# Kernel tuning notes

Measured on AMD Instinct MI355X. Metric: run time of the kernel, lower is better.

Reference implementation:

```python
import jax, jax.numpy as jnp
import numpy as np

B_SZ, T, D = 4, 8192, 512

def setup_inputs() -> dict:
    key = jax.random.key(0)
    k1, k2, k3, k4 = jax.random.split(key, 4)
    x = jax.random.normal(k1, (B_SZ, T, D), dtype=jnp.float32)
    # nn.Linear(dim, dim, bias=False) weights, applied as x @ W.T
    W_B = jax.random.normal(k2, (D, D), dtype=jnp.float32) * (1.0 / np.sqrt(D))
    W_C = jax.random.normal(k3, (D, D), dtype=jnp.float32) * (1.0 / np.sqrt(D))
    A = jax.random.normal(k4, (D,), dtype=jnp.float32)
    return {"x": x, "W_B": W_B, "W_C": W_C, "A": A}

def reference(x, W_B, W_C, A):
    # b: [B, T, D]
    b = jnp.einsum('btd,ed->bte', x, W_B)
    a = jax.nn.sigmoid(A)  # [D], diagonal decay per channel

    def step(h, b_t):
        h = a * h + b_t  # [B, D]
        return h, h

    h0 = jnp.zeros_like(b[:, 0])
    _, outs = jax.lax.scan(step, h0, jnp.swapaxes(b, 0, 1))  # outs: [T, B, D]
    outputs = jnp.swapaxes(outs, 0, 1)  # [B, T, D]
    return jnp.einsum('btd,ed->bte', outputs, W_C)
```

## Files before the change

kernel.cpp:

```cpp
#include <hip/hip_runtime.h>
#include <hip/hip_bf16.h>
#include <stdint.h>

#define B_SZ 4
#define T_LEN 8192
#define D_DIM 512
#define M_TOT 32768
#define RB 64
#define NCH 128
#define SCS 516

typedef __attribute__((ext_vector_type(8))) short bf16x8v;
typedef __attribute__((ext_vector_type(4))) float f32x4v;

__device__ __forceinline__ unsigned short f2bf(float f) {
  unsigned int u = __float_as_uint(f);
  u += 0x7fffu + ((u >> 16) & 1u);
  return (unsigned short)(u >> 16);
}
__device__ __forceinline__ float bf2f(unsigned short b) {
  return __uint_as_float(((unsigned int)b) << 16);
}
__device__ __forceinline__ float sigmoidf_(float x) { return 1.0f / (1.0f + expf(-x)); }

__device__ __forceinline__ bf16x8v pack8(float4 a, float4 b) {
  union { unsigned u[4]; bf16x8v v; } r;
  r.u[0] = (unsigned)f2bf(a.x) | ((unsigned)f2bf(a.y) << 16);
  r.u[1] = (unsigned)f2bf(a.z) | ((unsigned)f2bf(a.w) << 16);
  r.u[2] = (unsigned)f2bf(b.x) | ((unsigned)f2bf(b.y) << 16);
  r.u[3] = (unsigned)f2bf(b.z) | ((unsigned)f2bf(b.w) << 16);
  return r.v;
}

__global__ void prep_k(const float* __restrict__ Wb, const float* __restrict__ Wc,
                       const float* __restrict__ A, unsigned short* __restrict__ wpk,
                       unsigned short* __restrict__ papk) {
  const int b = blockIdx.x;
  const int tid = threadIdx.x;
  if (b == 64) {
#pragma unroll
    for (int s = 0; s < 2; ++s) {
      int ch = s * 256 + tid;
      float a = sigmoidf_(A[ch]);
      float p = a;
      int lhi = ((ch >> 3) & 3) << 4;
      int e = ch & 7;
      int csl = ch >> 5;
      for (int row = 0; row < RB; ++row) {
        int chunk = (row >> 4) * 16 + csl;
        int lane = (row & 15) | lhi;
        papk[chunk * 512 + lane * 8 + e] = f2bf(p);
        p *= a;
      }
    }
    return;
  }
  __shared__ unsigned short sd[16 * 520];
  const float* src = (b < 32) ? Wb + (size_t)b * 8192 : Wc + (size_t)(b - 32) * 8192;
  unsigned short* dst =
      (b < 32) ? wpk + (size_t)b * 8192 : wpk + 262144 + (size_t)(b - 32) * 8192;
#pragma unroll
  for (int it = 0; it < 4; ++it) {
    int idx = (it * 256 + tid) * 8;
    int row = idx >> 9, col = idx & 511;
    float4 v0 = *(const float4*)&src[row * 512 + col];
    float4 v1 = *(const float4*)&src[row * 512 + col + 4];
    uint4 o;
    o.x = (unsigned)f2bf(v0.x) | ((unsigned)f2bf(v0.y) << 16);
    o.y = (unsigned)f2bf(v0.z) | ((unsigned)f2bf(v0.w) << 16);
    o.z = (unsigned)f2bf(v1.x) | ((unsigned)f2bf(v1.y) << 16);
    o.w = (unsigned)f2bf(v1.z) | ((unsigned)f2bf(v1.w) << 16);
    *(uint4*)&sd[row * 520 + col] = o;
  }
  __syncthreads();
#pragma unroll
  for (int it = 0; it < 4; ++it) {
    int idx = it * 256 + tid;
    int cs = idx >> 6, l = idx & 63;
    uint4 v = *(const uint4*)&sd[(l & 15) * 520 + cs * 32 + (l >> 4) * 8];
    *(uint4*)&dst[(size_t)cs * 512 + l * 8] = v;
  }
}

__global__ void carry_k(const float* __restrict__ A, float* __restrict__ cst) {
  const int ch = threadIdx.x;
  const int bi = blockIdx.x;
  float a = sigmoidf_(A[ch]);
  float p = a;
#pragma unroll
  for (int i = 0; i < 6; ++i) p *= p;
  float H = 0.f;
  for (int cg = 0; cg < 16; ++cg) {
    float v[8];
    size_t base = ((size_t)bi * NCH + cg * 8) * 512 + ch;
#pragma unroll
    for (int i = 0; i < 8; ++i) v[i] = cst[base + (size_t)i * 512];
#pragma unroll
    for (int i = 0; i < 8; ++i) {
      float lf = v[i];
      cst[base + (size_t)i * 512] = H;
      H = fmaf(p, H, lf);
    }
  }
}

template <int MODE>
__global__ __launch_bounds__(512, 1) void gemm_k(
    const void* __restrict__ Aptr, const unsigned short* __restrict__ Bpk,
    float* __restrict__ C, const float* __restrict__ Ad,
    unsigned short* __restrict__ hOut, float* __restrict__ cst,
    const unsigned short* __restrict__ papk) {
  __shared__ union {
    float sc[RB * SCS];
    float tp[8][16 * 132];
  } sm;

  const int tid = threadIdx.x;
  const int lane = tid & 63;
  const int w = tid >> 6;
  const int wmi = w >> 2;
  const int wni = w & 3;
  const int mt = blockIdx.x;
  const int l15 = lane & 15;
  const int g4 = lane >> 4;

  const unsigned short* bB = Bpk + ((size_t)(wni * 8) * 16) * 512 + lane * 8;

  f32x4v acc[4][8] = {};

  if constexpr (MODE == 0) {
    const float* ax = (const float*)Aptr + (size_t)(mt * 128 + wmi * 64 + l15) * 512 + g4 * 8;
#pragma unroll 4
    for (int t = 0; t < 16; ++t) {
      bf16x8v af[4], bf_[8];
#pragma unroll
      for (int i = 0; i < 4; ++i) {
        float4 u0 = *(const float4*)&ax[(size_t)i * 8192 + t * 32];
        float4 u1 = *(const float4*)&ax[(size_t)i * 8192 + t * 32 + 4];
        af[i] = pack8(u0, u1);
      }
#pragma unroll
      for (int j = 0; j < 8; ++j)
        bf_[j] = *(const bf16x8v*)&bB[(size_t)j * 8192 + t * 512];
      __builtin_amdgcn_s_setprio(1);
#pragma unroll
      for (int i = 0; i < 4; ++i)
#pragma unroll
        for (int j = 0; j < 8; ++j)
          acc[i][j] = __builtin_amdgcn_mfma_f32_16x16x32_bf16(af[i], bf_[j], acc[i][j], 0, 0, 0);
      __builtin_amdgcn_s_setprio(0);
    }
  } else {
    const unsigned short* ah =
        (const unsigned short*)Aptr + ((size_t)(mt * 8 + wmi * 4) * 16) * 512 + lane * 8;
    const unsigned short* pa = papk + lane * 8;
    const float* cg = cst + (size_t)(mt * 2 + wmi) * 512 + g4 * 8;
#pragma unroll 4
    for (int t = 0; t < 16; ++t) {
      float4 c0 = *(const float4*)&cg[t * 32];
      float4 c1 = *(const float4*)&cg[t * 32 + 4];
      float cf[8] = {c0.x, c0.y, c0.z, c0.w, c1.x, c1.y, c1.z, c1.w};
      bf16x8v af[4], bf_[8];
#pragma unroll
      for (int i = 0; i < 4; ++i) {
        uint4 hv = *(const uint4*)&ah[(size_t)i * 8192 + t * 512];
        uint4 pv = *(const uint4*)&pa[(size_t)i * 8192 + t * 512];
        const unsigned* hw = (const unsigned*)&hv;
        const unsigned* pw = (const unsigned*)&pv;
        union { unsigned u[4]; bf16x8v v; } r;
#pragma unroll
        for (int q = 0; q < 4; ++q) {
          float o0 = fmaf(bf2f((unsigned short)(pw[q] & 0xffff)), cf[2 * q],
                          bf2f((unsigned short)(hw[q] & 0xffff)));
          float o1 = fmaf(bf2f((unsigned short)(pw[q] >> 16)), cf[2 * q + 1],
                          bf2f((unsigned short)(hw[q] >> 16)));
          r.u[q] = (unsigned)f2bf(o0) | ((unsigned)f2bf(o1) << 16);
        }
        af[i] = r.v;
      }
#pragma unroll
      for (int j = 0; j < 8; ++j)
        bf_[j] = *(const bf16x8v*)&bB[(size_t)j * 8192 + t * 512];
      __builtin_amdgcn_s_setprio(1);
#pragma unroll
      for (int i = 0; i < 4; ++i)
#pragma unroll
        for (int j = 0; j < 8; ++j)
          acc[i][j] = __builtin_amdgcn_mfma_f32_16x16x32_bf16(af[i], bf_[j], acc[i][j], 0, 0, 0);
      __builtin_amdgcn_s_setprio(0);
    }
  }

  if constexpr (MODE == 0) {
    float a2 = sigmoidf_(Ad[tid]);
#pragma unroll
    for (int c = 0; c < 2; ++c) {
      if (wmi == c) {
#pragma unroll
        for (int i = 0; i < 4; ++i)
#pragma unroll
          for (int j = 0; j < 8; ++j)
#pragma unroll
            for (int r = 0; r < 4; ++r)
              sm.sc[(i * 16 + g4 * 4 + r) * SCS + wni * 128 + j * 16 + l15] = acc[i][j][r];
      }
      __syncthreads();
      {
        float h = 0.f;
#pragma unroll 8
        for (int tt = 0; tt < RB; ++tt) {
          h = fmaf(a2, h, sm.sc[tt * SCS + tid]);
          sm.sc[tt * SCS + tid] = h;
        }
        cst[(size_t)(mt * 2 + c) * 512 + tid] = h;
      }
      __syncthreads();
#pragma unroll
      for (int p = 0; p < 8; ++p) {
        int idx = p * 512 + tid;
        int cl = idx >> 6, l = idx & 63;
        int rbl = cl >> 4, cs = cl & 15;
        const float* s = &sm.sc[(rbl * 16 + (l & 15)) * SCS + cs * 32 + (l >> 4) * 8];
        unsigned w0 = (unsigned)f2bf(s[0]) | ((unsigned)f2bf(s[1]) << 16);
        unsigned w1 = (unsigned)f2bf(s[2]) | ((unsigned)f2bf(s[3]) << 16);
        unsigned w2 = (unsigned)f2bf(s[4]) | ((unsigned)f2bf(s[5]) << 16);
        unsigned w3 = (unsigned)f2bf(s[6]) | ((unsigned)f2bf(s[7]) << 16);
        *(uint4*)&hOut[(((size_t)(mt * 2 + c) * 4 + rbl) * 16 + cs) * 512 + l * 8] =
            make_uint4(w0, w1, w2, w3);
      }
      __syncthreads();
    }
  } else {
    float* tp = sm.tp[w];
#pragma unroll
    for (int i = 0; i < 4; ++i) {
#pragma unroll
      for (int j = 0; j < 8; ++j)
#pragma unroll
        for (int r = 0; r < 4; ++r)
          tp[(g4 * 4 + r) * 132 + j * 16 + l15] = acc[i][j][r];
#pragma unroll
      for (int p = 0; p < 8; ++p) {
        int row = p * 2 + (lane >> 5);
        int slot = lane & 31;
        f32x4v v = *(const f32x4v*)&tp[row * 132 + slot * 4];
        *(f32x4v*)&C[(size_t)(mt * 128 + wmi * 64 + i * 16 + row) * 512 + wni * 128 + slot * 4] =
            v;
      }
    }
  }
}

extern "C" void kernel_launch(void* const* d_in, const int* in_sizes, int n_in,
                              void* d_out, int out_size, void* d_ws, size_t ws_size,
                              hipStream_t stream) {
  const float* x = (const float*)d_in[0];
  const float* W_B = (const float*)d_in[1];
  const float* W_C = (const float*)d_in[2];
  const float* A = (const float*)d_in[3];
  float* out = (float*)d_out;
  char* ws = (char*)d_ws;

  unsigned short* Wpk = (unsigned short*)ws;
  unsigned short* papk = (unsigned short*)(ws + 0x100000);
  float* cst = (float*)(ws + 0x120000);
  unsigned short* hpk = (unsigned short*)(ws + 0x220000);

  prep_k<<<65, 256, 0, stream>>>(W_B, W_C, A, Wpk, papk);

  gemm_k<0><<<256, 512, 0, stream>>>(x, Wpk, nullptr, A, hpk, cst, nullptr);
  carry_k<<<B_SZ, 512, 0, stream>>>(A, cst);
  gemm_k<1><<<256, 512, 0, stream>>>(hpk, Wpk + 262144, out, nullptr, nullptr, cst, papk);
}
```

Baseline: 96.45 us.

## Double-buffer GEMM global loads with inline asm and explicit vmcnt waits

Replaces the simple per-k-step load-then-MFMA loops in both GEMM modes with a software-pipelined double buffer. Global loads for step t+1 are issued via inline asm before computing step t, with s_waitcnt vmcnt and sched_barrier controlling ordering. This is meant to hide global memory latency behind MFMA work. It doubles register usage for staged operands, which may lower occupancy. It also depends on hand-counted vmcnt values being correct, since the compiler cannot track the asm loads.

```diff
diff --git a/kernel.cpp b/kernel.cpp
--- a/kernel.cpp
+++ b/kernel.cpp
@@ -12,6 +12,7 @@
 
 typedef __attribute__((ext_vector_type(8))) short bf16x8v;
 typedef __attribute__((ext_vector_type(4))) float f32x4v;
+typedef __attribute__((ext_vector_type(4))) unsigned int u32x4v;
 
 __device__ __forceinline__ unsigned short f2bf(float f) {
   unsigned int u = __float_as_uint(f);
@@ -23,7 +24,7 @@
 }
 __device__ __forceinline__ float sigmoidf_(float x) { return 1.0f / (1.0f + expf(-x)); }
 
-__device__ __forceinline__ bf16x8v pack8(float4 a, float4 b) {
+__device__ __forceinline__ bf16x8v pack8v(f32x4v a, f32x4v b) {
   union { unsigned u[4]; bf16x8v v; } r;
   r.u[0] = (unsigned)f2bf(a.x) | ((unsigned)f2bf(a.y) << 16);
   r.u[1] = (unsigned)f2bf(a.z) | ((unsigned)f2bf(a.w) << 16);
@@ -31,6 +32,8 @@
   r.u[3] = (unsigned)f2bf(b.z) | ((unsigned)f2bf(b.w) << 16);
   return r.v;
 }
+
+#define GLD(d, p) asm volatile("global_load_dwordx4 %0, %1, off" : "=v"(d) : "v"(p))
 
 __global__ void prep_k(const float* __restrict__ Wb, const float* __restrict__ Wc,
                        const float* __restrict__ A, unsigned short* __restrict__ wpk,
@@ -130,65 +133,109 @@
 
   if constexpr (MODE == 0) {
     const float* ax = (const float*)Aptr + (size_t)(mt * 128 + wmi * 64 + l15) * 512 + g4 * 8;
-#pragma unroll 4
-    for (int t = 0; t < 16; ++t) {
-      bf16x8v af[4], bf_[8];
-#pragma unroll
-      for (int i = 0; i < 4; ++i) {
-        float4 u0 = *(const float4*)&ax[(size_t)i * 8192 + t * 32];
-        float4 u1 = *(const float4*)&ax[(size_t)i * 8192 + t * 32 + 4];
-        af[i] = pack8(u0, u1);
-      }
-#pragma unroll
-      for (int j = 0; j < 8; ++j)
-        bf_[j] = *(const bf16x8v*)&bB[(size_t)j * 8192 + t * 512];
-      __builtin_amdgcn_s_setprio(1);
-#pragma unroll
-      for (int i = 0; i < 4; ++i)
-#pragma unroll
-        for (int j = 0; j < 8; ++j)
-          acc[i][j] = __builtin_amdgcn_mfma_f32_16x16x32_bf16(af[i], bf_[j], acc[i][j], 0, 0, 0);
-      __builtin_amdgcn_s_setprio(0);
-    }
+    f32x4v a0[8], a1[8];
+    u32x4v b0[8], b1[8];
+#define ISS0(ab, bb, t)                                              \
+  {                                                                  \
+    _Pragma("unroll") for (int i = 0; i < 4; ++i) {                  \
+      GLD(ab[2 * i], ax + (size_t)i * 8192 + (t) * 32);              \
+      GLD(ab[2 * i + 1], ax + (size_t)i * 8192 + (t) * 32 + 4);      \
+    }                                                                \
+    _Pragma("unroll") for (int j = 0; j < 8; ++j)                    \
+      GLD(bb[j], bB + (size_t)j * 8192 + (t) * 512);                 \
+  }
+#define CMP0(ab, bb)                                                 \
+  {                                                                  \
+    bf16x8v af[4];                                                   \
+    _Pragma("unroll") for (int i = 0; i < 4; ++i)                    \
+      af[i] = pack8v(ab[2 * i], ab[2 * i + 1]);                      \
+    __builtin_amdgcn_s_setprio(1);                                   \
+    _Pragma("unroll") for (int i = 0; i < 4; ++i)                    \
+      _Pragma("unroll") for (int j = 0; j < 8; ++j)                  \
+        acc[i][j] = __builtin_amdgcn_mfma_f32_16x16x32_bf16(         \
+            af[i], *(const bf16x8v*)&bb[j], acc[i][j], 0, 0, 0);     \
+    __builtin_amdgcn_s_setprio(0);                                   \
+  }
+    ISS0(a0, b0, 0);
+#pragma unroll
+    for (int t = 0; t < 16; t += 2) {
+      ISS0(a1, b1, t + 1);
+      asm volatile("s_waitcnt vmcnt(16)");
+      __builtin_amdgcn_sched_barrier(0);
+      CMP0(a0, b0);
+      if (t + 2 < 16) {
+        ISS0(a0, b0, t + 2);
+        asm volatile("s_waitcnt vmcnt(16)");
+      } else {
+        asm volatile("s_waitcnt vmcnt(0)");
+      }
+      __builtin_amdgcn_sched_barrier(0);
+      CMP0(a1, b1);
+    }
+#undef ISS0
+#undef CMP0
   } else {
     const unsigned short* ah =
         (const unsigned short*)Aptr + ((size_t)(mt * 8 + wmi * 4) * 16) * 512 + lane * 8;
     const unsigned short* pa = papk + lane * 8;
     const float* cg = cst + (size_t)(mt * 2 + wmi) * 512 + g4 * 8;
-#pragma unroll 4
-    for (int t = 0; t < 16; ++t) {
-      float4 c0 = *(const float4*)&cg[t * 32];
-      float4 c1 = *(const float4*)&cg[t * 32 + 4];
-      float cf[8] = {c0.x, c0.y, c0.z, c0.w, c1.x, c1.y, c1.z, c1.w};
-      bf16x8v af[4], bf_[8];
-#pragma unroll
-      for (int i = 0; i < 4; ++i) {
-        uint4 hv = *(const uint4*)&ah[(size_t)i * 8192 + t * 512];
-        uint4 pv = *(const uint4*)&pa[(size_t)i * 8192 + t * 512];
-        const unsigned* hw = (const unsigned*)&hv;
-        const unsigned* pw = (const unsigned*)&pv;
-        union { unsigned u[4]; bf16x8v v; } r;
-#pragma unroll
-        for (int q = 0; q < 4; ++q) {
-          float o0 = fmaf(bf2f((unsigned short)(pw[q] & 0xffff)), cf[2 * q],
-                          bf2f((unsigned short)(hw[q] & 0xffff)));
-          float o1 = fmaf(bf2f((unsigned short)(pw[q] >> 16)), cf[2 * q + 1],
-                          bf2f((unsigned short)(hw[q] >> 16)));
-          r.u[q] = (unsigned)f2bf(o0) | ((unsigned)f2bf(o1) << 16);
-        }
-        af[i] = r.v;
-      }
-#pragma unroll
-      for (int j = 0; j < 8; ++j)
-        bf_[j] = *(const bf16x8v*)&bB[(size_t)j * 8192 + t * 512];
-      __builtin_amdgcn_s_setprio(1);
-#pragma unroll
-      for (int i = 0; i < 4; ++i)
-#pragma unroll
-        for (int j = 0; j < 8; ++j)
-          acc[i][j] = __builtin_amdgcn_mfma_f32_16x16x32_bf16(af[i], bf_[j], acc[i][j], 0, 0, 0);
-      __builtin_amdgcn_s_setprio(0);
-    }
+    u32x4v h0[4], h1[4], p0[4], p1[4];
+    f32x4v c0[2], c1[2];
+    u32x4v b0[8], b1[8];
+#define ISS1(hb, pb, cb, bb, t)                                      \
+  {                                                                  \
+    _Pragma("unroll") for (int i = 0; i < 4; ++i) {                  \
+      GLD(hb[i], ah + (size_t)i * 8192 + (t) * 512);                 \
+      GLD(pb[i], pa + (size_t)i * 8192 + (t) * 512);                 \
+    }                                                                \
+    GLD(cb[0], cg + (t) * 32);                                       \
+    GLD(cb[1], cg + (t) * 32 + 4);                                   \
+    _Pragma("unroll") for (int j = 0; j < 8; ++j)                    \
+      GLD(bb[j], bB + (size_t)j * 8192 + (t) * 512);                 \
+  }
+#define CMP1(hb, pb, cb, bb)                                              \
+  {                                                                       \
+    float cf[8] = {cb[0].x, cb[0].y, cb[0].z, cb[0].w,                    \
+                   cb[1].x, cb[1].y, cb[1].z, cb[1].w};                   \
+    bf16x8v af[4];                                                        \
+    _Pragma("unroll") for (int i = 0; i < 4; ++i) {                       \
+      const unsigned* hw = (const unsigned*)&hb[i];                       \
+      const unsigned* pw = (const unsigned*)&pb[i];                       \
+      union { unsigned u[4]; bf16x8v v; } r;                              \
+      _Pragma("unroll") for (int q = 0; q < 4; ++q) {                     \
+        float o0 = fmaf(bf2f((unsigned short)(pw[q] & 0xffff)), cf[2 * q],\
+                        bf2f((unsigned short)(hw[q] & 0xffff)));          \
+        float o1 = fmaf(bf2f((unsigned short)(pw[q] >> 16)), cf[2 * q + 1],\
+                        bf2f((unsigned short)(hw[q] >> 16)));             \
+        r.u[q] = (unsigned)f2bf(o0) | ((unsigned)f2bf(o1) << 16);         \
+      }                                                                   \
+      af[i] = r.v;                                                        \
+    }                                                                     \
+    __builtin_amdgcn_s_setprio(1);                                        \
+    _Pragma("unroll") for (int i = 0; i < 4; ++i)                         \
+      _Pragma("unroll") for (int j = 0; j < 8; ++j)                       \
+        acc[i][j] = __builtin_amdgcn_mfma_f32_16x16x32_bf16(              \
+            af[i], *(const bf16x8v*)&bb[j], acc[i][j], 0, 0, 0);          \
+    __builtin_amdgcn_s_setprio(0);                                        \
+  }
+    ISS1(h0, p0, c0, b0, 0);
+#pragma unroll
+    for (int t = 0; t < 16; t += 2) {
+      ISS1(h1, p1, c1, b1, t + 1);
+      asm volatile("s_waitcnt vmcnt(18)");
+      __builtin_amdgcn_sched_barrier(0);
+      CMP1(h0, p0, c0, b0);
+      if (t + 2 < 16) {
+        ISS1(h0, p0, c0, b0, t + 2);
+        asm volatile("s_waitcnt vmcnt(18)");
+      } else {
+        asm volatile("s_waitcnt vmcnt(0)");
+      }
+      __builtin_amdgcn_sched_barrier(0);
+      CMP1(h1, p1, c1, b1);
+    }
+#undef ISS1
+#undef CMP1
   }
 
   if constexpr (MODE == 0) {
```

New measurement: 202.1 us. 109% more time.
